# Performance work log

Measured on AMD Instinct MI355X. Metric: run time of the kernel, lower is better.

The kernel has to match this reference:

```python
import jax, jax.numpy as jnp
import numpy as np

# ---- config derived from init_kwargs ----
D_MODEL = 768
QK = 64            # qk_dim
HEADDIM = 64
D_INNER = 1536     # round(2.0 * d_model)
H = D_INNER // HEADDIM  # 24 heads
NUM_BC = 2         # share_BC_for_two_graphs -> 4 - 2
NUM_DT = 2         # share_dt_for_two_graphs -> 4 - 2
D_IN_PROJ = 2 * D_INNER + QK * 2 * NUM_BC + H * 2 * NUM_DT  # 3424
CONV_DIM = D_INNER + QK * 2 * NUM_BC                        # 1792
IH, IW = 32, 32
EPS = 1e-5


def setup_inputs() -> dict:
    key = jax.random.key(0)
    ks = jax.random.split(key, 4)
    Bsz, L = 32, IH * IW
    return {
        "u": jax.random.normal(ks[0], (Bsz, L, D_MODEL), jnp.float32),
        "w_in": jax.random.normal(ks[1], (D_IN_PROJ, D_MODEL), jnp.float32) * 0.02,
        "conv_w": jax.random.normal(ks[2], (CONV_DIM, 1, 3, 3), jnp.float32) * 0.1,
        "conv_b": jnp.zeros((CONV_DIM,), jnp.float32),
        "norm_w": jnp.ones((D_INNER,), jnp.float32),
        "w_out": jax.random.normal(ks[3], (D_MODEL, D_INNER), jnp.float32) * 0.02,
    }


def _ssm_scan(dt, Bm, Cm, x):
    """Selective scan. dt:(b,L,H)  Bm,Cm:(b,L,N)  x:(b,L,H,P) -> y:(b,L,H,P)"""
    a = jnp.exp(-dt)  # per-step decay (A = -1 per head)

    def step(h, inp):
        a_t, dt_t, B_t, C_t, x_t = inp
        h = a_t[:, :, None, None] * h + jnp.einsum('bh,bn,bhp->bhnp', dt_t, B_t, x_t)
        y = jnp.einsum('bn,bhnp->bhp', C_t, h)
        return h, y

    b, _, nh = dt.shape
    N, P = Bm.shape[-1], x.shape[-1]
    h0 = jnp.zeros((b, nh, N, P), dt.dtype)
    mv = lambda t: jnp.moveaxis(t, 1, 0)  # put L in scan position
    _, ys = jax.lax.scan(step, h0, (mv(a), mv(dt), mv(Bm), mv(Cm), mv(x)))
    return jnp.moveaxis(ys, 0, 1)


def reference(u, w_in, conv_w, conv_b, norm_w, w_out):
    b, L, _ = u.shape
    zxBCdt = u @ w_in.T  # (b, L, D_IN_PROJ)
    z, xBC, dt = jnp.split(
        zxBCdt, [D_INNER, 2 * D_INNER + QK * 2 * NUM_BC], axis=-1)

    # depthwise 3x3 conv2d over the (IH, IW) token grid, NCHW layout
    x4 = jnp.moveaxis(xBC.reshape(b, IH, IW, CONV_DIM), 3, 1)
    x4 = jax.lax.conv_general_dilated(
        x4, conv_w, window_strides=(1, 1), padding=[(1, 1), (1, 1)],
        feature_group_count=CONV_DIM)
    x4 = jax.nn.silu(x4 + conv_b[None, :, None, None])
    xBC = jnp.moveaxis(x4, 1, 3).reshape(b, L, CONV_DIM)

    x, Bc, Cc = jnp.split(xBC, [D_INNER, D_INNER + NUM_BC * QK], axis=-1)
    xh = x.reshape(b, L, H, HEADDIM)
    Bc = Bc.reshape(b, L, NUM_BC, QK)
    Cc = Cc.reshape(b, L, NUM_BC, QK)
    # dt: 2 graphs x 2 directions, each per-head
    dt_all = jax.nn.softplus(dt.reshape(b, L, 2 * NUM_DT, H))

    y = jnp.zeros((b, L, H, HEADDIM), u.dtype)
    for k in range(2 * NUM_DT):       # fixed small loop: graph x direction
        g, rev = k // 2, k % 2
        dtk, Bk, Ck, xk = dt_all[:, :, k], Bc[:, :, g], Cc[:, :, g], xh
        if rev:  # backward direction over the token sequence
            dtk, Bk, Ck, xk = (jnp.flip(t, 1) for t in (dtk, Bk, Ck, xk))
        yk = _ssm_scan(dtk, Bk, Ck, xk)
        y = y + (jnp.flip(yk, 1) if rev else yk)

    y = y.reshape(b, L, D_INNER)
    # gated RMSNorm (Mamba2-style): norm(y * silu(z)) * weight
    yg = y * jax.nn.silu(z)
    yn = yg * jax.lax.rsqrt(jnp.mean(yg * yg, axis=-1, keepdims=True) + EPS)
    yn = yn * norm_w
    return yn @ w_out.T  # (b, L, d_model)
```

## Files before the change

### kernel.cpp

```cpp
#include <hip/hip_runtime.h>
#include <hip/hip_bf16.h>
#include <stdint.h>


#define D_MODEL 768
#define D_INNER 1536
#define NH 24
#define D_IN_PROJ 3424
#define CONV_DIM 1792
#define NDT 96
#define LSEQ 1024

typedef __bf16 bf16x8 __attribute__((ext_vector_type(8)));
typedef float f32x4 __attribute__((ext_vector_type(4)));

__global__ void cvt_kernel(const float* __restrict__ src, __hip_bfloat16* __restrict__ dst, int n4) {
    int i = blockIdx.x * 256 + threadIdx.x;
    if (i < n4) {
        float4 v = ((const float4*)src)[i];
        __hip_bfloat162 lo, hi;
        lo.x = __float2bfloat16(v.x); lo.y = __float2bfloat16(v.y);
        hi.x = __float2bfloat16(v.z); hi.y = __float2bfloat16(v.w);
        ((__hip_bfloat162*)dst)[2*i]   = lo;
        ((__hip_bfloat162*)dst)[2*i+1] = hi;
    }
}

__global__ void repack_w(const float* __restrict__ cw, float* __restrict__ wT) {
    int i = blockIdx.x * 256 + threadIdx.x;
    if (i < CONV_DIM * 9) {
        int c = i / 9, t = i % 9;
        wT[t * CONV_DIM + c] = cw[i];
    }
}

__device__ __forceinline__ void gl_lds16(const __hip_bfloat16* g, __hip_bfloat16* l) {
    __builtin_amdgcn_global_load_lds(
        (const __attribute__((address_space(1))) void*)g,
        (__attribute__((address_space(3))) void*)l, 16, 0, 0);
}

template<int MODE>
__global__ __launch_bounds__(256) void gemm_bt(
    const __hip_bfloat16* __restrict__ A,
    const __hip_bfloat16* __restrict__ Bt,
    float* __restrict__ OutF,
    __hip_bfloat16* __restrict__ Z, __hip_bfloat16* __restrict__ XBC, float* __restrict__ DT,
    int M, int N, int K)
{
    __shared__ __hip_bfloat16 As[128*32];
    __shared__ __hip_bfloat16 Bs[128*32];
    const int tid  = threadIdx.x;
    const int wave = tid >> 6, lane = tid & 63;
    const int bm = blockIdx.x * 128, bn = blockIdx.y * 128;
    const int wm = (wave >> 1) * 64, wn = (wave & 1) * 64;
    f32x4 acc[4][4] = {};
    const int lrow = lane >> 2;
    const int lcol = (lane & 3) * 8;
    const int fr = lane & 15, fk = (lane >> 4) * 8;
    const int ktiles = K >> 5;
    for (int kt = 0; kt < ktiles; ++kt) {
        const int kofs = kt * 32;
        #pragma unroll
        for (int cc = 0; cc < 2; ++cc) {
            int r = (wave*2 + cc)*16 + lrow;
            gl_lds16(A + (size_t)(bm + r)*K + kofs + lcol, &As[r*32 + lcol]);
            int gn = bn + r; if (gn > N-1) gn = N-1;
            gl_lds16(Bt + (size_t)gn*K + kofs + lcol, &Bs[r*32 + lcol]);
        }
        __syncthreads();
        bf16x8 af[4], bfr[4];
        #pragma unroll
        for (int i = 0; i < 4; ++i)
            af[i] = *reinterpret_cast<const bf16x8*>(&As[(wm + i*16 + fr)*32 + fk]);
        #pragma unroll
        for (int j = 0; j < 4; ++j)
            bfr[j] = *reinterpret_cast<const bf16x8*>(&Bs[(wn + j*16 + fr)*32 + fk]);
        #pragma unroll
        for (int i = 0; i < 4; ++i)
            #pragma unroll
            for (int j = 0; j < 4; ++j)
                acc[i][j] = __builtin_amdgcn_mfma_f32_16x16x32_bf16(af[i], bfr[j], acc[i][j], 0, 0, 0);
        __syncthreads();
    }
    const int er = (lane >> 4) * 4;
    const int ec = lane & 15;
    #pragma unroll
    for (int i = 0; i < 4; ++i) {
        #pragma unroll
        for (int j = 0; j < 4; ++j) {
            #pragma unroll
            for (int r = 0; r < 4; ++r) {
                int row = bm + wm + i*16 + er + r;
                int col = bn + wn + j*16 + ec;
                if (col < N) {
                    float v = acc[i][j][r];
                    if (MODE == 0) {
                        OutF[(size_t)row*N + col] = v;
                    } else {
                        if (col < D_INNER)
                            Z[(size_t)row*D_INNER + col] = __float2bfloat16(v);
                        else if (col < 3328)
                            XBC[(size_t)row*CONV_DIM + (col - D_INNER)] = __float2bfloat16(v);
                        else
                            DT[(size_t)row*NDT + (col - 3328)] = v;
                    }
                }
            }
        }
    }
}

__global__ __launch_bounds__(256) void conv_kernel(
    const __hip_bfloat16* __restrict__ xbc,
    const float* __restrict__ wT,
    const float* __restrict__ cb,
    __hip_bfloat16* __restrict__ out)
{
    size_t idx = (size_t)blockIdx.x * 256 + threadIdx.x;
    const int cg = (int)(idx % (CONV_DIM / 8));
    const int c = cg * 8;
    size_t bp = idx / (CONV_DIM / 8);
    const int pix = (int)(bp % LSEQ);
    const int b = (int)(bp / LSEQ);
    const int y = pix >> 5, x = pix & 31;
    float acc[8];
    {
        float4 c0 = *(const float4*)(cb + c);
        float4 c1 = *(const float4*)(cb + c + 4);
        acc[0]=c0.x; acc[1]=c0.y; acc[2]=c0.z; acc[3]=c0.w;
        acc[4]=c1.x; acc[5]=c1.y; acc[6]=c1.z; acc[7]=c1.w;
    }
    const size_t rowbase = (size_t)b * LSEQ;
    #pragma unroll
    for (int dy = -1; dy <= 1; ++dy) {
        int yy = y + dy; if (yy < 0 || yy > 31) continue;
        #pragma unroll
        for (int dx = -1; dx <= 1; ++dx) {
            int xx = x + dx; if (xx < 0 || xx > 31) continue;
            const int t = (dy+1)*3 + (dx+1);
            bf16x8 v = *(const bf16x8*)(xbc + (rowbase + yy*32 + xx)*(size_t)CONV_DIM + c);
            float4 w0 = *(const float4*)(wT + t*CONV_DIM + c);
            float4 w1 = *(const float4*)(wT + t*CONV_DIM + c + 4);
            acc[0] += w0.x * (float)v[0];
            acc[1] += w0.y * (float)v[1];
            acc[2] += w0.z * (float)v[2];
            acc[3] += w0.w * (float)v[3];
            acc[4] += w1.x * (float)v[4];
            acc[5] += w1.y * (float)v[5];
            acc[6] += w1.z * (float)v[6];
            acc[7] += w1.w * (float)v[7];
        }
    }
    bf16x8 o;
    #pragma unroll
    for (int i = 0; i < 8; ++i) {
        float s = acc[i] / (1.f + __expf(-acc[i]));
        o[i] = (__bf16)s;
    }
    *(bf16x8*)(out + (rowbase + pix)*(size_t)CONV_DIM + c) = o;
}

#define SW(r) ((((r) & 7) ^ (((r) >> 3) & 7)) << 3)
__device__ __forceinline__ f32x4 mfma16(bf16x8 a, bf16x8 b, f32x4 c) {
    return __builtin_amdgcn_mfma_f32_16x16x32_bf16(a, b, c, 0, 0, 0);
}
__device__ __forceinline__ void bar_lds() {
    asm volatile("s_waitcnt lgkmcnt(0)" ::: "memory");
    __builtin_amdgcn_s_barrier();
    __builtin_amdgcn_sched_barrier(0);
}

__global__ __launch_bounds__(256, 2) void scan_ssd(
    const __bf16* __restrict__ conv,
    const float* __restrict__ dtraw,
    __bf16* __restrict__ yf,
    __bf16* __restrict__ yr)
{
    const int tid = threadIdx.x;
    const int w = tid >> 6, lane = tid & 63;
    const int b = blockIdx.x, h = blockIdx.y, dir = blockIdx.z;
    __bf16* yout = dir ? yr : yf;
    const size_t base = (size_t)b * LSEQ;
    const size_t Rtot = (size_t)gridDim.x * LSEQ;

    __shared__ __align__(16) __bf16 XT[64*64];
    __shared__ __align__(16) __bf16 Gs[64*64];
    __shared__ __align__(16) __bf16 Ts[2][64*64];
    __shared__ __align__(16) __bf16 Bss[2][64*64];
    __shared__ __align__(16) __bf16 HT[2][64*64];
    __shared__ float Warr[2][2][64], Earr[2][2][64], Wmarr[2][2][64], Rmarr[2][2][64];

    f32x4 Hst0[4] = {}, Hst1[4] = {};

    const int srow = tid >> 2;
    const int scol = (tid & 3) * 16;
    const int fr = lane & 15, fkq = (lane >> 4) * 8;
    const int er = (lane >> 4) * 4, ec = lane & 15;
    const int rn = w*16 + fr;
    const int sl = dir ? 63 - srow : srow;
    const int swsl = SW(sl);
    const int swrn = SW(rn);

    const int rA0 = dir ? (LSEQ - 64) : 0;
    const ptrdiff_t dRow = (ptrdiff_t)(dir ? -64 : 64) * CONV_DIM;
    const ptrdiff_t dDt  = (ptrdiff_t)(dir ? -64 : 64) * NDT;
    const __bf16* pRow = conv + (base + rA0 + srow) * (size_t)CONV_DIM;
    const __bf16* pC   = conv + (base + rA0 + (dir ? 63 - rn : rn)) * (size_t)CONV_DIM + 1664;
    const float*  pDt  = dtraw + (base + rA0 + (dir ? 63 - lane : lane)) * NDT
                         + (2*(tid >> 6) + dir)*24 + h;
    const int xoff = h*64 + scol;

    float pfdN = 0.f;
    if (tid < 128) {
        const int g = tid >> 6;
        float d0 = *pDt;
        float e = __expf(d0);
        float dts = __logf(1.f + e);
        float s = dts;
        #pragma unroll
        for (int off = 1; off < 64; off <<= 1) {
            float v = __shfl_up(s, off, 64);
            if (lane >= off) s += v;
        }
        float stot = __shfl(s, 63, 64);
        float smid = __shfl(s, 31, 64);
        Warr[0][g][lane]  = __expf(s - stot) * dts;
        Earr[0][g][lane]  = __expf(-s);
        Wmarr[0][g][lane] = __expf(s - smid) * dts;
        Rmarr[0][g][lane] = __expf(smid - s);
        pDt += dDt;
        pfdN = *pDt;
    }
    bf16x8 pfx0 = *(const bf16x8*)(pRow + xoff);
    bf16x8 pfx1 = *(const bf16x8*)(pRow + xoff + 8);
    bf16x8 pfb00 = *(const bf16x8*)(pRow + 1536 + scol);
    bf16x8 pfb01 = *(const bf16x8*)(pRow + 1536 + scol + 8);
    bf16x8 pfb10 = *(const bf16x8*)(pRow + 1600 + scol);
    bf16x8 pfb11 = *(const bf16x8*)(pRow + 1600 + scol + 8);
    bf16x8 pfc00 = *(const bf16x8*)(pC + fkq);
    bf16x8 pfc01 = *(const bf16x8*)(pC + 32 + fkq);
    bf16x8 pfc10 = *(const bf16x8*)(pC + 64 + fkq);
    bf16x8 pfc11 = *(const bf16x8*)(pC + 96 + fkq);
    bar_lds();

    #pragma unroll 1
    for (int c = 0; c < 16; ++c) {
        const int cb = c & 1;
        const int rA = dir ? (LSEQ - (c+1)*64) : c*64;

        const bf16x8 c00 = pfc00, c01 = pfc01, c10 = pfc10, c11 = pfc11;

        {
            #pragma unroll
            for (int i = 0; i < 8; ++i) {
                const int p = scol + i;
                XT[p*64 + (sl ^ SW(p))] = pfx0[i];
            }
            #pragma unroll
            for (int i = 0; i < 8; ++i) {
                const int p = scol + 8 + i;
                XT[p*64 + (sl ^ SW(p))] = pfx1[i];
            }
        }
        {
            const float ws0 = Warr[cb][0][sl];
            const float ws1 = Warr[cb][1][sl];
            #pragma unroll
            for (int i = 0; i < 8; ++i) {
                const int n = scol + i;
                Ts[0][n*64 + (sl ^ SW(n))] = (__bf16)((float)pfb00[i] * ws0);
                Ts[1][n*64 + (sl ^ SW(n))] = (__bf16)((float)pfb10[i] * ws1);
            }
            #pragma unroll
            for (int i = 0; i < 8; ++i) {
                const int n = scol + 8 + i;
                Ts[0][n*64 + (sl ^ SW(n))] = (__bf16)((float)pfb01[i] * ws0);
                Ts[1][n*64 + (sl ^ SW(n))] = (__bf16)((float)pfb11[i] * ws1);
            }
            *(bf16x8*)&Bss[0][sl*64 + (scol ^ swsl)]       = pfb00;
            *(bf16x8*)&Bss[0][sl*64 + ((scol + 8) ^ swsl)] = pfb01;
            *(bf16x8*)&Bss[1][sl*64 + (scol ^ swsl)]       = pfb10;
            *(bf16x8*)&Bss[1][sl*64 + ((scol + 8) ^ swsl)] = pfb11;
        }
        {
            #pragma unroll
            for (int t4 = 0; t4 < 4; ++t4) {
                const int p = t4*16 + ec;
                const int swp = SW(p);
                #pragma unroll
                for (int j = 0; j < 2; ++j) {
                    const int n = w*16 + er + 2*j;
                    __hip_bfloat162 pr0, pr1;
                    pr0.x = __float2bfloat16(Hst0[t4][2*j]);
                    pr0.y = __float2bfloat16(Hst0[t4][2*j+1]);
                    pr1.x = __float2bfloat16(Hst1[t4][2*j]);
                    pr1.y = __float2bfloat16(Hst1[t4][2*j+1]);
                    *(__hip_bfloat162*)&HT[0][p*64 + (n ^ swp)] = pr0;
                    *(__hip_bfloat162*)&HT[1][p*64 + (n ^ swp)] = pr1;
                }
            }
        }
        {
            const float e630 = Earr[cb][0][63];
            const float e631 = Earr[cb][1][63];
            #pragma unroll
            for (int t4 = 0; t4 < 4; ++t4)
                #pragma unroll
                for (int rr = 0; rr < 4; ++rr) {
                    Hst0[t4][rr] *= e630;
                    Hst1[t4][rr] *= e631;
                }
        }
        if (c < 15 && tid < 128) {
            const int g = tid >> 6;
            float e = __expf(pfdN);
            float dts = __logf(1.f + e);
            float s = dts;
            #pragma unroll
            for (int off = 1; off < 64; off <<= 1) {
                float v = __shfl_up(s, off, 64);
                if (lane >= off) s += v;
            }
            float stot = __shfl(s, 63, 64);
            float smid = __shfl(s, 31, 64);
            const int nb = cb ^ 1;
            Warr[nb][g][lane]  = __expf(s - stot) * dts;
            Earr[nb][g][lane]  = __expf(-s);
            Wmarr[nb][g][lane] = __expf(s - smid) * dts;
            Rmarr[nb][g][lane] = __expf(smid - s);
        }
        if (c != 15) {
            pRow += dRow; pC += dRow;
            pfx0 = *(const bf16x8*)(pRow + xoff);
            pfx1 = *(const bf16x8*)(pRow + xoff + 8);
            pfb00 = *(const bf16x8*)(pRow + 1536 + scol);
            pfb01 = *(const bf16x8*)(pRow + 1536 + scol + 8);
            pfb10 = *(const bf16x8*)(pRow + 1600 + scol);
            pfb11 = *(const bf16x8*)(pRow + 1600 + scol + 8);
            pfc00 = *(const bf16x8*)(pC + fkq);
            pfc01 = *(const bf16x8*)(pC + 32 + fkq);
            pfc10 = *(const bf16x8*)(pC + 64 + fkq);
            pfc11 = *(const bf16x8*)(pC + 96 + fkq);
            if (c < 14 && tid < 128) { pDt += dDt; pfdN = *pDt; }
        }
        bar_lds();

        bf16x8 cf[2][2] = { { c00, c01 }, { c10, c11 } };
        bf16x8 ga[2][2], ca[2][2], ta[2][2];
        #pragma unroll
        for (int g = 0; g < 2; ++g) {
            f32x4 Gacc[4] = {};
            __builtin_amdgcn_s_setprio(1);
            #pragma unroll
            for (int s4 = 0; s4 < 4; ++s4) {
                const int s = s4*16 + fr;
                const int ss = SW(s);
                bf16x8 bb0 = *(const bf16x8*)&Bss[g][s*64 + (fkq ^ ss)];
                bf16x8 bb1 = *(const bf16x8*)&Bss[g][s*64 + ((32 + fkq) ^ ss)];
                Gacc[s4] = mfma16(cf[g][0], bb0, Gacc[s4]);
                Gacc[s4] = mfma16(cf[g][1], bb1, Gacc[s4]);
            }
            __builtin_amdgcn_s_setprio(0);
            float rmv[4];
            #pragma unroll
            for (int rr = 0; rr < 4; ++rr) rmv[rr] = Rmarr[cb][g][w*16 + er + rr];
            #pragma unroll
            for (int s4 = 0; s4 < 4; ++s4) {
                const int s = s4*16 + ec;
                const float wm = Wmarr[cb][g][s];
                #pragma unroll
                for (int rr = 0; rr < 4; ++rr) {
                    const int tau = w*16 + er + rr;
                    float m = (tau >= s) ? wm * rmv[rr] : 0.f;
                    Gs[tau*64 + (s ^ SW(tau))] = (__bf16)(Gacc[s4][rr] * m);
                }
            }
            ga[g][0] = *(const bf16x8*)&Gs[rn*64 + (fkq ^ swrn)];
            ga[g][1] = *(const bf16x8*)&Gs[rn*64 + ((32 + fkq) ^ swrn)];
            const float esc = Earr[cb][g][rn];
            #pragma unroll
            for (int i = 0; i < 8; ++i) {
                ca[g][0][i] = (__bf16)((float)cf[g][0][i] * esc);
                ca[g][1][i] = (__bf16)((float)cf[g][1][i] * esc);
            }
            ta[g][0] = *(const bf16x8*)&Ts[g][rn*64 + (fkq ^ swrn)];
            ta[g][1] = *(const bf16x8*)&Ts[g][rn*64 + ((32 + fkq) ^ swrn)];
        }
        f32x4 Yacc[4] = {};
        __builtin_amdgcn_s_setprio(1);
        #pragma unroll
        for (int p4 = 0; p4 < 4; ++p4) {
            const int p = p4*16 + fr;
            const int sp = SW(p);
            bf16x8 x0  = *(const bf16x8*)&XT[p*64 + (fkq ^ sp)];
            bf16x8 x1  = *(const bf16x8*)&XT[p*64 + ((32 + fkq) ^ sp)];
            bf16x8 h00 = *(const bf16x8*)&HT[0][p*64 + (fkq ^ sp)];
            bf16x8 h01 = *(const bf16x8*)&HT[0][p*64 + ((32 + fkq) ^ sp)];
            bf16x8 h10 = *(const bf16x8*)&HT[1][p*64 + (fkq ^ sp)];
            bf16x8 h11 = *(const bf16x8*)&HT[1][p*64 + ((32 + fkq) ^ sp)];
            Yacc[p4] = mfma16(ga[0][0], x0, Yacc[p4]);
            Yacc[p4] = mfma16(ga[0][1], x1, Yacc[p4]);
            Yacc[p4] = mfma16(ca[0][0], h00, Yacc[p4]);
            Yacc[p4] = mfma16(ca[0][1], h01, Yacc[p4]);
            Yacc[p4] = mfma16(ga[1][0], x0, Yacc[p4]);
            Yacc[p4] = mfma16(ga[1][1], x1, Yacc[p4]);
            Yacc[p4] = mfma16(ca[1][0], h10, Yacc[p4]);
            Yacc[p4] = mfma16(ca[1][1], h11, Yacc[p4]);
            Hst0[p4] = mfma16(ta[0][0], x0, Hst0[p4]);
            Hst0[p4] = mfma16(ta[0][1], x1, Hst0[p4]);
            Hst1[p4] = mfma16(ta[1][0], x0, Hst1[p4]);
            Hst1[p4] = mfma16(ta[1][1], x1, Hst1[p4]);
        }
        __builtin_amdgcn_s_setprio(0);

        #pragma unroll
        for (int p4 = 0; p4 < 4; ++p4)
            #pragma unroll
            for (int rr = 0; rr < 4; ++rr) {
                const int tau = w*16 + er + rr;
                Gs[tau*64 + ((p4*16 + ec) ^ SW(tau))] = (__bf16)Yacc[p4][rr];
            }
        bar_lds();
        {
            const int rowp = rA + (dir ? 63 - srow : srow);
            bf16x8 y0 = *(const bf16x8*)&Gs[srow*64 + (scol ^ SW(srow))];
            bf16x8 y1 = *(const bf16x8*)&Gs[srow*64 + ((scol + 8) ^ SW(srow))];
            __bf16* dst = yout + ((size_t)h * Rtot + (base + rowp)) * 64 + scol;
            *(bf16x8*)dst = y0;
            *(bf16x8*)(dst + 8) = y1;
        }
    }
}

__global__ __launch_bounds__(256) void gate_kernel(
    const __hip_bfloat16* __restrict__ yf, const __hip_bfloat16* __restrict__ yr,
    const __hip_bfloat16* __restrict__ z, const float* __restrict__ norm_w,
    __hip_bfloat16* __restrict__ yn)
{
    const int row = blockIdx.x, tid = threadIdx.x;
    const size_t R = gridDim.x;
    const size_t ybase = (size_t)row * D_INNER;
    float yg[6]; float ss = 0.f;
    #pragma unroll
    for (int k = 0; k < 6; ++k) {
        int j = tid + k*256;
        size_t yidx = ((size_t)(j >> 6) * R + row) * 64 + (j & 63);
        float yv = __bfloat162float(yf[yidx]) + __bfloat162float(yr[yidx]);
        float zz = __bfloat162float(z[ybase+j]);
        float g  = yv * (zz / (1.f + __expf(-zz)));
        yg[k] = g; ss += g*g;
    }
    #pragma unroll
    for (int off = 32; off > 0; off >>= 1) ss += __shfl_down(ss, off, 64);
    __shared__ float red[4];
    if ((tid & 63) == 0) red[tid >> 6] = ss;
    __syncthreads();
    float total = red[0] + red[1] + red[2] + red[3];
    float rn = rsqrtf(total * (1.f/1536.f) + 1e-5f);
    #pragma unroll
    for (int k = 0; k < 6; ++k) {
        int j = tid + k*256;
        yn[ybase+j] = __float2bfloat16(yg[k] * rn * norm_w[j]);
    }
}

extern "C" void kernel_launch(void* const* d_in, const int* in_sizes, int n_in,
                              void* d_out, int out_size, void* d_ws, size_t ws_size,
                              hipStream_t stream) {
    const float* u      = (const float*)d_in[0];
    const float* w_in   = (const float*)d_in[1];
    const float* conv_w = (const float*)d_in[2];
    const float* conv_b = (const float*)d_in[3];
    const float* norm_w = (const float*)d_in[4];
    const float* w_out  = (const float*)d_in[5];
    (void)in_sizes; (void)n_in; (void)out_size;

    char* ws = (char*)d_ws;
    const size_t nWin  = (size_t)D_IN_PROJ * D_MODEL;
    const size_t nWout = (size_t)D_MODEL * D_INNER;
    __hip_bfloat16* win_bf  = (__hip_bfloat16*)ws;
    __hip_bfloat16* wout_bf = (__hip_bfloat16*)(ws + nWin*2);
    float* wT = (float*)(ws + nWin*2 + nWout*2);
    const size_t wbytes = nWin*2 + nWout*2 + (size_t)9*CONV_DIM*4;
    char* arena = ws + wbytes;

    const size_t perRow = 10624;
    int CB = 32;
    while (CB > 1 && wbytes + perRow*(size_t)CB*1024 > ws_size) CB >>= 1;
    const int nchunks = 32 / CB;
    const size_t R = (size_t)CB * 1024;

    __hip_bfloat16* segA = (__hip_bfloat16*)arena;
    char* pC = arena + R*3072;
    char* pD = pC + R*3584;
    char* pE = pD + R*384;
    __hip_bfloat16* xbc_bf  = (__hip_bfloat16*)pC;
    __hip_bfloat16* yr_bf   = (__hip_bfloat16*)pC;
    float*          dt_f32  = (float*)pD;
    __hip_bfloat16* conv_bf = (__hip_bfloat16*)pE;
    __hip_bfloat16* yn_bf   = (__hip_bfloat16*)pE;
    __hip_bfloat16* u_bf    = segA;
    __hip_bfloat16* yf_bf   = segA;

    cvt_kernel<<<(int)((nWin/4 + 255)/256), 256, 0, stream>>>(w_in, win_bf, (int)(nWin/4));
    cvt_kernel<<<(int)((nWout/4 + 255)/256), 256, 0, stream>>>(w_out, wout_bf, (int)(nWout/4));
    repack_w<<<(CONV_DIM*9 + 255)/256, 256, 0, stream>>>(conv_w, wT);

    for (int c = 0; c < nchunks; ++c) {
        const float* u_c = u + (size_t)c * R * D_MODEL;
        __hip_bfloat16* z_bf = (__hip_bfloat16*)((char*)d_out + (size_t)c * R * 3072);
        float* out_c = (float*)d_out + (size_t)c * R * D_MODEL;

        const size_t nUc4 = R * D_MODEL / 4;
        cvt_kernel<<<(int)((nUc4 + 255)/256), 256, 0, stream>>>(u_c, u_bf, (int)nUc4);

        gemm_bt<1><<<dim3((int)(R/128), (D_IN_PROJ + 127)/128), 256, 0, stream>>>(
            u_bf, win_bf, nullptr, z_bf, xbc_bf, dt_f32, (int)R, D_IN_PROJ, D_MODEL);

        conv_kernel<<<(int)((R*(CONV_DIM/8))/256), 256, 0, stream>>>(xbc_bf, wT, conv_b, conv_bf);

        scan_ssd<<<dim3(CB, NH, 2), 256, 0, stream>>>(
            (const __bf16*)conv_bf, dt_f32, (__bf16*)yf_bf, (__bf16*)yr_bf);

        gate_kernel<<<(int)R, 256, 0, stream>>>(yf_bf, yr_bf, z_bf, norm_w, yn_bf);

        gemm_bt<0><<<dim3((int)(R/128), D_MODEL/128), 256, 0, stream>>>(
            yn_bf, wout_bf, out_c, nullptr, nullptr, nullptr, (int)R, D_MODEL, D_INNER);
    }
}
```

Baseline: 1.040 ms.

## Use BK=64 tiles with XOR-swizzled LDS and XCD-aware block remap in GEMM

Raises the GEMM K-tile from 32 to 64, which halves the number of barrier pairs per K loop and doubles the MFMA work done per LDS fill. The global-to-LDS loads use an XOR swizzle on the column to avoid LDS bank conflicts on the 128-byte row stride. The block index is also remapped so consecutive blocks on the same XCD share M rows, aiming for better L2 reuse. The remap assumes gridDim.x is a multiple of 8 and that M and K divide evenly. LDS use doubles, which may lower occupancy.

```diff
diff --git a/kernel.cpp b/kernel.cpp
--- a/kernel.cpp
+++ b/kernel.cpp
@@ -48,39 +48,51 @@
     __hip_bfloat16* __restrict__ Z, __hip_bfloat16* __restrict__ XBC, float* __restrict__ DT,
     int M, int N, int K)
 {
-    __shared__ __hip_bfloat16 As[128*32];
-    __shared__ __hip_bfloat16 Bs[128*32];
+    __shared__ __hip_bfloat16 As[128*64];
+    __shared__ __hip_bfloat16 Bs[128*64];
     const int tid  = threadIdx.x;
     const int wave = tid >> 6, lane = tid & 63;
-    const int bm = blockIdx.x * 128, bn = blockIdx.y * 128;
+    const int nbm = gridDim.x, nbn = gridDim.y;
+    const int d = blockIdx.y * nbm + blockIdx.x;
+    const int bmPerX = nbm >> 3;
+    const int jj = d >> 3;
+    const int bm = ((d & 7) * bmPerX + jj / nbn) * 128;
+    const int bn = (jj % nbn) * 128;
     const int wm = (wave >> 1) * 64, wn = (wave & 1) * 64;
     f32x4 acc[4][4] = {};
-    const int lrow = lane >> 2;
-    const int lcol = (lane & 3) * 8;
-    const int fr = lane & 15, fk = (lane >> 4) * 8;
-    const int ktiles = K >> 5;
+    const int srow8 = tid >> 3;
+    const int scol8 = (tid & 7) * 8;
+    const int swzw = (srow8 & 7) << 3;
+    const int fr = lane & 15, fkq = (lane >> 4) * 8;
+    const int swzr = (fr & 7) << 3;
+    const int ktiles = K >> 6;
     for (int kt = 0; kt < ktiles; ++kt) {
-        const int kofs = kt * 32;
-        #pragma unroll
-        for (int cc = 0; cc < 2; ++cc) {
-            int r = (wave*2 + cc)*16 + lrow;
-            gl_lds16(A + (size_t)(bm + r)*K + kofs + lcol, &As[r*32 + lcol]);
+        const int kofs = kt * 64;
+        #pragma unroll
+        for (int cc = 0; cc < 4; ++cc) {
+            const int r = cc*32 + srow8;
+            const int sc = kofs + (scol8 ^ swzw);
+            gl_lds16(A + (size_t)(bm + r)*K + sc, &As[r*64 + scol8]);
             int gn = bn + r; if (gn > N-1) gn = N-1;
-            gl_lds16(Bt + (size_t)gn*K + kofs + lcol, &Bs[r*32 + lcol]);
+            gl_lds16(Bt + (size_t)gn*K + sc, &Bs[r*64 + scol8]);
         }
         __syncthreads();
-        bf16x8 af[4], bfr[4];
-        #pragma unroll
-        for (int i = 0; i < 4; ++i)
-            af[i] = *reinterpret_cast<const bf16x8*>(&As[(wm + i*16 + fr)*32 + fk]);
-        #pragma unroll
-        for (int j = 0; j < 4; ++j)
-            bfr[j] = *reinterpret_cast<const bf16x8*>(&Bs[(wn + j*16 + fr)*32 + fk]);
-        #pragma unroll
-        for (int i = 0; i < 4; ++i)
+        #pragma unroll
+        for (int kk = 0; kk < 2; ++kk) {
+            const int fks = (kk*32 + fkq) ^ swzr;
+            bf16x8 af[4], bfr[4];
+            #pragma unroll
+            for (int i = 0; i < 4; ++i)
+                af[i] = *reinterpret_cast<const bf16x8*>(&As[(wm + i*16 + fr)*64 + fks]);
             #pragma unroll
             for (int j = 0; j < 4; ++j)
-                acc[i][j] = __builtin_amdgcn_mfma_f32_16x16x32_bf16(af[i], bfr[j], acc[i][j], 0, 0, 0);
+                bfr[j] = *reinterpret_cast<const bf16x8*>(&Bs[(wn + j*16 + fr)*64 + fks]);
+            #pragma unroll
+            for (int i = 0; i < 4; ++i)
+                #pragma unroll
+                for (int j = 0; j < 4; ++j)
+                    acc[i][j] = __builtin_amdgcn_mfma_f32_16x16x32_bf16(af[i], bfr[j], acc[i][j], 0, 0, 0);
+        }
         __syncthreads();
     }
     const int er = (lane >> 4) * 4;
```

Result: slower. 1.088 ms (+4.6%).
